# Kernel optimization log

Measured on AMD Instinct MI355X. Metric: run time of the kernel, lower is better.

Reference implementation:

```python
import jax, jax.numpy as jnp
import numpy as np

B, N, C_IN, C_OUT, K = 8, 4096, 64, 128, 15
RADIUS = 0.1            # 2.5 * grid_size(0.04) * sigma(1.0)
MAX_NN = 34
KP_EXTENT = 0.04        # point_influence = prev_grid_size * sigma
KERNEL_RADIUS = 1.5 * KP_EXTENT
NEG_SLOPE = 0.2
BN_EPS = 1e-5


def setup_inputs() -> dict:
    key = jax.random.key(0)
    k1, k2, k3, k4 = jax.random.split(key, 4)
    xyz = jax.random.uniform(k1, (B, N, 3), dtype=jnp.float32)
    feats = jax.random.normal(k2, (B, N, C_IN), dtype=jnp.float32)
    # fixed kernel point disposition inside the kernel ball (requires_grad=False in torch)
    kp = jax.random.normal(k3, (K, 3), dtype=jnp.float32)
    kp = kp / (jnp.linalg.norm(kp, axis=-1, keepdims=True) + 1e-6) * KERNEL_RADIUS * 0.7
    kp = kp.at[0].set(0.0)  # center point
    std = float(np.sqrt(2.0 / (K * C_IN)))
    weight = jax.random.normal(k4, (K, C_IN, C_OUT), dtype=jnp.float32) * std
    gamma = jnp.ones((C_OUT,), dtype=jnp.float32)
    beta = jnp.zeros((C_OUT,), dtype=jnp.float32)
    return {"xyz": xyz, "feats": feats, "K_points": kp, "weight": weight,
            "gamma": gamma, "beta": beta}


def _ball_query(xyz):
    # xyz: [B, N, 3] -> flat neighbor idx [B*N, MAX_NN] into the concatenated
    # point array; missing neighbors get shadow index B*N.
    b_, n_, _ = xyz.shape
    shadow = b_ * n_

    def per_cloud(pts, b):
        d2 = jnp.sum((pts[:, None, :] - pts[None, :, :]) ** 2, axis=-1)  # [N, N]
        neg_d2, idx = jax.lax.top_k(-d2, MAX_NN)                         # k nearest
        valid = (-neg_d2) <= RADIUS ** 2
        return jnp.where(valid, idx + b * n_, shadow)

    return jax.vmap(per_cloud)(xyz, jnp.arange(b_)).reshape(b_ * n_, MAX_NN)


def _kpconv_block(xyz, feats, K_points, weight, gamma, beta):
    b_, n_, _ = xyz.shape
    pts = xyz.reshape(b_ * n_, 3)
    f = feats.reshape(b_ * n_, C_IN)
    nidx = _ball_query(xyz)                                   # [M, nn]
    # shadow point far away / zero features (KPConv_ops)
    pts_pad = jnp.concatenate([pts, jnp.full((1, 3), 1e6, pts.dtype)], axis=0)
    f_pad = jnp.concatenate([f, jnp.zeros((1, C_IN), f.dtype)], axis=0)
    nbr = pts_pad[nidx] - pts[:, None, :]                     # [M, nn, 3] relative coords
    sq = jnp.sum((nbr[:, :, None, :] - K_points) ** 2, -1)    # [M, nn, K]
    w = jnp.maximum(1.0 - jnp.sqrt(sq) / KP_EXTENT, 0.0)      # linear influence
    nf = f_pad[nidx]                                          # [M, nn, Cin]
    wf = jnp.einsum('mnk,mnc->mkc', w, nf)                    # per-kernel-point feats
    out = jnp.einsum('mkc,kcd->md', wf, weight)               # [M, Cout]
    # FastBatchNorm1d (training-mode batch stats, biased var) + LeakyReLU
    mu = out.mean(axis=0)
    var = out.var(axis=0)
    out = (out - mu) * jax.lax.rsqrt(var + BN_EPS) * gamma + beta
    out = jnp.where(out >= 0, out, NEG_SLOPE * out)
    return out.reshape(b_, n_, C_OUT)


def reference(xyz, feats, K_points, weight, gamma, beta):
    return _kpconv_block(xyz, feats, K_points, weight, gamma, beta)
```

## Files before the change

kernel.cpp:

```cpp
#include <hip/hip_runtime.h>


#define NB     8
#define NPTS   4096
#define M_TOT  32768
#define CIN    64
#define COUT   128
#define NKP    15
#define NCELL  1728
#define UCAP   400
#define R2EFF  (0.082f * 0.082f)
#define KP_INV 25.0f
#define NEG_SLOPE 0.2f
#define KCP    960
#define WFROW  1920
#define SP     40

typedef float f32x4_t __attribute__((ext_vector_type(4)));
typedef short bf16x8_t __attribute__((ext_vector_type(8)));

__device__ __forceinline__ unsigned short f2bf(float f) {
  union { float f; unsigned u; } v; v.f = f;
  unsigned r = v.u + 0x7FFF + ((v.u >> 16) & 1);
  return (unsigned short)(r >> 16);
}
__device__ __forceinline__ unsigned short f2bf_fast(float f) {
  union { float f; unsigned u; } v; v.f = f;
  return (unsigned short)((v.u + 0x8000u) >> 16);
}
__device__ __forceinline__ int cell_of(float x, float y, float z) {
  int cx = (int)(x * 12.f); cx = cx > 11 ? 11 : cx;
  int cy = (int)(y * 12.f); cy = cy > 11 ? 11 : cy;
  int cz = (int)(z * 12.f); cz = cz > 11 ? 11 : cz;
  return (cz * 12 + cy) * 12 + cx;
}

__global__ __launch_bounds__(256) void k0a_hist(
    const float* __restrict__ xyz, int* __restrict__ cellcnt)
{
  const int pt = blockIdx.x * 256 + threadIdx.x;
  const float x = xyz[pt * 3], y = xyz[pt * 3 + 1], z = xyz[pt * 3 + 2];
  const int b = pt >> 12;
  atomicAdd(&cellcnt[b * NCELL + cell_of(x, y, z)], 1);
}

__global__ __launch_bounds__(256) void k0b_scan_kW(
    const int* __restrict__ cellcnt, int* __restrict__ cellstart,
    const float* __restrict__ W, unsigned short* __restrict__ Wt)
{
  if (blockIdx.x >= 8) {
    const int idx = (blockIdx.x - 8) * 256 + threadIdx.x;
    const int c = idx & 63, d = idx >> 6;
    #pragma unroll
    for (int k = 0; k < NKP; k++)
      Wt[(size_t)d * KCP + k * 64 + c] =
          f2bf(W[(size_t)k * (CIN * COUT) + c * COUT + d]);
    return;
  }
  __shared__ int ps[256];
  const int b = blockIdx.x, t = threadIdx.x;
  int local[7], s = 0;
  #pragma unroll
  for (int i = 0; i < 7; i++) {
    const int cid = t * 7 + i;
    const int c = (cid < NCELL) ? cellcnt[b * NCELL + cid] : 0;
    local[i] = c; s += c;
  }
  ps[t] = s; __syncthreads();
  for (int off = 1; off < 256; off <<= 1) {
    int v = (t >= off) ? ps[t - off] : 0;
    __syncthreads();
    ps[t] += v;
    __syncthreads();
  }
  int run = ps[t] - s;
  #pragma unroll
  for (int i = 0; i < 7; i++) {
    const int cid = t * 7 + i;
    if (cid < NCELL) { cellstart[b * 1729 + cid] = run; run += local[i]; }
  }
  if (t == 255) cellstart[b * 1729 + NCELL] = ps[255];
}

__global__ __launch_bounds__(256) void k0c_scatter(
    const float* __restrict__ xyz, const float* __restrict__ feats,
    const int* __restrict__ cellstart, int* __restrict__ cellfill,
    int* __restrict__ qorder, float4* __restrict__ xyzs,
    unsigned short* __restrict__ fsorted)
{
  const int pt = blockIdx.x * 256 + threadIdx.x;
  const float x = xyz[pt * 3], y = xyz[pt * 3 + 1], z = xyz[pt * 3 + 2];
  const int b = pt >> 12;
  const int cid = cell_of(x, y, z);
  const int slot = atomicAdd(&cellfill[b * NCELL + cid], 1);
  const int pos = b * NPTS + cellstart[b * 1729 + cid] + slot;
  qorder[pos] = pt;
  xyzs[pos] = make_float4(x, y, z, 0.f);
  const float* src = &feats[(size_t)pt * CIN];
  uint4* dst = (uint4*)&fsorted[(size_t)pos * CIN];
  #pragma unroll
  for (int g = 0; g < 8; g++) {
    float4 a = *(const float4*)(src + g * 8);
    float4 c = *(const float4*)(src + g * 8 + 4);
    union { unsigned short s[8]; uint4 v; } u;
    u.s[0] = f2bf(a.x); u.s[1] = f2bf(a.y); u.s[2] = f2bf(a.z); u.s[3] = f2bf(a.w);
    u.s[4] = f2bf(c.x); u.s[5] = f2bf(c.y); u.s[6] = f2bf(c.z); u.s[7] = f2bf(c.w);
    dst[g] = u.v;
  }
}

__global__ __launch_bounds__(256, 5) void k2_conv(
    const float4* __restrict__ xyzs, const unsigned short* __restrict__ fsorted,
    const float* __restrict__ kpts, const int* __restrict__ cellstart,
    const int* __restrict__ qorder, const unsigned short* __restrict__ Wt,
    float* __restrict__ out, float* __restrict__ psum,
    float* __restrict__ psumsq)
{
  __shared__ char smraw[32000] __attribute__((aligned(16)));
  float4*         Pu   = (float4*)smraw;
  unsigned short* cpos = (unsigned short*)(smraw + 6400);
  short (*S)[SP]       = (short(*)[SP])(smraw + 6400);
  short (*FT)[SP]      = (short(*)[SP])(smraw + 26880);

  __shared__ float4 qd[16];
  __shared__ int    qm[16];
  __shared__ float  kp[NKP][4];
  __shared__ int    Tsh;
  __shared__ int    ucnt;

  const int tid = threadIdx.x;
  const int w   = tid >> 6;
  const int L   = tid & 63;
  const int m0  = blockIdx.x * 16;
  const int b   = m0 >> 12;

  if (tid >= 64 && tid < 64 + NKP) {
    const int k = tid - 64;
    const float kx = kpts[k * 3], ky = kpts[k * 3 + 1], kz = kpts[k * 3 + 2];
    kp[k][0] = -2.f * kx; kp[k][1] = -2.f * ky; kp[k][2] = -2.f * kz;
    kp[k][3] = kx * kx + ky * ky + kz * kz;
  }

  if (tid < 64) {
    int cxm = 12, cym = 12, czm = 12, cxM = -1, cyM = -1, czM = -1;
    if (tid < 16) {
      const float4 Q = xyzs[m0 + tid];
      qd[tid] = Q;
      qm[tid] = qorder[m0 + tid];
      int a = (int)(Q.x * 12.f); a = a > 11 ? 11 : a;
      int c = (int)(Q.y * 12.f); c = c > 11 ? 11 : c;
      int d = (int)(Q.z * 12.f); d = d > 11 ? 11 : d;
      cxm = cxM = a; cym = cyM = c; czm = czM = d;
    }
    #pragma unroll
    for (int off = 8; off >= 1; off >>= 1) {
      int v;
      v = __shfl_xor(cxm, off); cxm = v < cxm ? v : cxm;
      v = __shfl_xor(cxM, off); cxM = v > cxM ? v : cxM;
      v = __shfl_xor(cym, off); cym = v < cym ? v : cym;
      v = __shfl_xor(cyM, off); cyM = v > cyM ? v : cyM;
      v = __shfl_xor(czm, off); czm = v < czm ? v : czm;
      v = __shfl_xor(czM, off); czM = v > czM ? v : czM;
    }
    cxm = __shfl(cxm, 0); cxM = __shfl(cxM, 0);
    cym = __shfl(cym, 0); cyM = __shfl(cyM, 0);
    czm = __shfl(czm, 0); czM = __shfl(czM, 0);

    const int x0 = cxm > 0 ? cxm - 1 : 0, x1 = cxM < 11 ? cxM + 1 : 11;
    const int y0 = cym > 0 ? cym - 1 : 0, y1 = cyM < 11 ? cyM + 1 : 11;
    const int z0 = czm > 0 ? czm - 1 : 0, z1 = czM < 11 ? czM + 1 : 11;
    const int yspan = y1 - y0 + 1;
    int nr = yspan * (z1 - z0 + 1);
    nr = nr > 64 ? 64 : nr;

    int rs = 0, len = 0;
    if (tid < nr) {
      const int zz = z0 + tid / yspan, yy = y0 + tid % yspan;
      const int base = b * 1729 + (zz * 12 + yy) * 12;
      rs  = cellstart[base + x0];
      len = cellstart[base + x1 + 1] - rs;
    }
    int incl = len;
    #pragma unroll
    for (int off = 1; off < 64; off <<= 1) {
      const int v = __shfl_up(incl, off);
      if (tid >= off) incl += v;
    }
    const int excl = incl - len;
    for (int i = 0; i < len; i++) cpos[excl + i] = (unsigned short)(rs + i);
    if (tid == 63) Tsh = incl;
    if (tid == 62) ucnt = 0;
  }
  __syncthreads();
  const int T = Tsh;

  for (int tb = 0; tb < T; tb += 256) {
    const int t = tb + tid;
    if (t < T) {
      const int pos = (int)cpos[t];
      const float4 P = xyzs[b * NPTS + pos];
      float best = 1e9f;
      #pragma unroll
      for (int i = 0; i < 16; i++) {
        const float4 Q = qd[i];
        const float dx = P.x - Q.x, dy = P.y - Q.y, dz = P.z - Q.z;
        const float d2 = dx * dx + dy * dy + dz * dz;
        best = d2 < best ? d2 : best;
      }
      if (best <= R2EFF) {
        const int slot = atomicAdd(&ucnt, 1);
        if (slot < UCAP)
          Pu[slot] = make_float4(P.x, P.y, P.z, __int_as_float(pos));
      }
    }
  }
  __syncthreads();
  int U = ucnt; U = U > UCAP ? UCAP : U;

  const int ln = L & 15;
  const int kh = L >> 4;
  const int qh = tid >> 5;
  const int nn = tid & 31;

  f32x4_t acc[16];
  #pragma unroll
  for (int mt = 0; mt < 16; mt++) acc[mt] = (f32x4_t){0.f, 0.f, 0.f, 0.f};

  for (int ub = 0; ub < U; ub += 32) {
    {
      const int c  = tid & 63;
      const int i0 = tid >> 6;
      #pragma unroll
      for (int ii = 0; ii < 8; ii++) {
        const int i = ii * 4 + i0;
        const int u = ub + i;
        short v = 0;
        if (u < U) {
          const int pos = __float_as_int(Pu[u].w);
          v = (short)fsorted[(size_t)(b * NPTS + pos) * CIN + c];
        }
        FT[c][i] = v;
      }
    }

    bf16x8_t bb;
    #pragma unroll
    for (int half = 0; half < 2; half++) {
      {
        const int u = ub + nn;
        if (u < U) {
          const float4 P = Pu[u];
          const float4 Q = qd[half * 8 + qh];
          const float rx = P.x - Q.x, ry = P.y - Q.y, rz = P.z - Q.z;
          const float rr = rx * rx + ry * ry + rz * rz;
          #pragma unroll
          for (int k = 0; k < NKP; k++) {
            float d2 = fmaf(kp[k][0], rx,
                       fmaf(kp[k][1], ry,
                       fmaf(kp[k][2], rz, rr + kp[k][3])));
            d2 = fmaxf(d2, 0.f);
            const float wv =
                fmaxf(fmaf(-KP_INV, __builtin_amdgcn_sqrtf(d2), 1.f), 0.f);
            S[qh * 16 + k][nn] = (short)f2bf_fast(wv);
          }
          S[qh * 16 + 15][nn] = 0;
        } else {
          #pragma unroll
          for (int k = 0; k < 16; k++) S[qh * 16 + k][nn] = 0;
        }
      }
      __syncthreads();
      if (half == 0) bb = *(const bf16x8_t*)&FT[w * 16 + ln][kh * 8];
      #pragma unroll
      for (int mt = 0; mt < 8; mt++) {
        bf16x8_t aa = *(const bf16x8_t*)&S[mt * 16 + ln][kh * 8];
        acc[half * 8 + mt] =
            __builtin_amdgcn_mfma_f32_16x16x32_bf16(aa, bb, acc[half * 8 + mt],
                                                    0, 0, 0);
      }
      __syncthreads();
    }
  }

  {
    const int c = w * 16 + ln;
    #pragma unroll
    for (int mt = 0; mt < 16; mt++) {
      #pragma unroll
      for (int j = 0; j < 4; j++) {
        const int k = kh * 4 + j;
        if (k < 15) {
          int byteo = mt * WFROW + ((k * 64 + c) << 1);
          byteo ^= (mt & 7) << 4;
          *(unsigned short*)(smraw + byteo) = f2bf_fast(acc[mt][j]);
        }
      }
    }
  }
  __syncthreads();

  const int colbase = w * 32;

  f32x4_t acc2[2];
  acc2[0] = (f32x4_t){0.f, 0.f, 0.f, 0.f};
  acc2[1] = (f32x4_t){0.f, 0.f, 0.f, 0.f};

  const unsigned short* Bp0 = &Wt[(size_t)(colbase + ln) * KCP + kh * 8];
  const unsigned short* Bp1 = Bp0 + 16 * KCP;
  const char* wfb = (const char*)smraw + ln * WFROW;
  const int   sw  = (ln & 7) << 4;

  #pragma unroll 6
  for (int kk = 0; kk < 30; kk++) {
    const int ko  = kk * 32;
    const int inr = (kh * 16 + kk * 64) ^ sw;
    bf16x8_t b0 = *(const bf16x8_t*)(Bp0 + ko);
    bf16x8_t b1 = *(const bf16x8_t*)(Bp1 + ko);
    bf16x8_t a0 = *(const bf16x8_t*)(wfb + inr);
    acc2[0] = __builtin_amdgcn_mfma_f32_16x16x32_bf16(a0, b0, acc2[0], 0, 0, 0);
    acc2[1] = __builtin_amdgcn_mfma_f32_16x16x32_bf16(a0, b1, acc2[1], 0, 0, 0);
  }

  float s0 = 0.f, q0 = 0.f, s1 = 0.f, q1 = 0.f;
  #pragma unroll
  for (int j = 0; j < 4; j++) {
    s0 += acc2[0][j]; q0 += acc2[0][j] * acc2[0][j];
    s1 += acc2[1][j]; q1 += acc2[1][j] * acc2[1][j];
  }
  s0 += __shfl_xor(s0, 16); s0 += __shfl_xor(s0, 32);
  q0 += __shfl_xor(q0, 16); q0 += __shfl_xor(q0, 32);
  s1 += __shfl_xor(s1, 16); s1 += __shfl_xor(s1, 32);
  q1 += __shfl_xor(q1, 16); q1 += __shfl_xor(q1, 32);
  if (kh == 0) {
    atomicAdd(&psum[colbase + ln], s0);
    atomicAdd(&psumsq[colbase + ln], q0);
    atomicAdd(&psum[colbase + 16 + ln], s1);
    atomicAdd(&psumsq[colbase + 16 + ln], q1);
  }

  #pragma unroll
  for (int c = 0; c < 2; c++) {
    #pragma unroll
    for (int j = 0; j < 4; j++) {
      const int row = kh * 4 + j;
      out[(size_t)qm[row] * COUT + colbase + c * 16 + ln] = acc2[c][j];
    }
  }
}

__global__ __launch_bounds__(256) void k4_norm(
    float* __restrict__ out, const float* __restrict__ psum,
    const float* __restrict__ psumsq, const float* __restrict__ gamma,
    const float* __restrict__ beta)
{
  __shared__ float a_s[128], b_s[128];
  if (threadIdx.x < 128) {
    const int d = threadIdx.x;
    double mu  = (double)psum[d] / (double)M_TOT;
    double var = (double)psumsq[d] / (double)M_TOT - mu * mu;
    float rstd = (float)(1.0 / sqrt(var + 1e-5));
    float a = rstd * gamma[d];
    a_s[d] = a;
    b_s[d] = beta[d] - (float)mu * a;
  }
  __syncthreads();
  const int idx = blockIdx.x * 256 + threadIdx.x;
  float4 v = ((const float4*)out)[idx];
  const int d0 = (idx * 4) & 127;
  float y0 = v.x * a_s[d0 + 0] + b_s[d0 + 0];
  float y1 = v.y * a_s[d0 + 1] + b_s[d0 + 1];
  float y2 = v.z * a_s[d0 + 2] + b_s[d0 + 2];
  float y3 = v.w * a_s[d0 + 3] + b_s[d0 + 3];
  v.x = y0 >= 0.f ? y0 : NEG_SLOPE * y0;
  v.y = y1 >= 0.f ? y1 : NEG_SLOPE * y1;
  v.z = y2 >= 0.f ? y2 : NEG_SLOPE * y2;
  v.w = y3 >= 0.f ? y3 : NEG_SLOPE * y3;
  ((float4*)out)[idx] = v;
}

extern "C" void kernel_launch(void* const* d_in, const int* in_sizes, int n_in,
                              void* d_out, int out_size, void* d_ws,
                              size_t ws_size, hipStream_t stream)
{
  const float* xyz   = (const float*)d_in[0];
  const float* feats = (const float*)d_in[1];
  const float* kpts  = (const float*)d_in[2];
  const float* W     = (const float*)d_in[3];
  const float* gamma = (const float*)d_in[4];
  const float* beta  = (const float*)d_in[5];
  float* out = (float*)d_out;

  char* ws = (char*)d_ws;
  int*            cellcnt   = (int*)(ws + 0);
  int*            cellfill  = (int*)(ws + 55296);
  float*          psum      = (float*)(ws + 110592);
  float*          psumsq    = (float*)(ws + 111104);
  int*            cellstart = (int*)(ws + 111616);
  int*            qorder    = (int*)(ws + 167040);
  float4*         xyzs      = (float4*)(ws + 298112);
  unsigned short* fsorted   = (unsigned short*)(ws + 822400);
  unsigned short* Wt        = (unsigned short*)(ws + 5016704);

  hipMemsetAsync(ws, 0, 111616, stream);

  k0a_hist   <<< 128, 256, 0, stream>>>(xyz, cellcnt);
  k0b_scan_kW<<<  40, 256, 0, stream>>>(cellcnt, cellstart, W, Wt);
  k0c_scatter<<< 128, 256, 0, stream>>>(xyz, feats, cellstart, cellfill,
                                        qorder, xyzs, fsorted);
  k2_conv    <<<2048, 256, 0, stream>>>(xyzs, fsorted, kpts, cellstart,
                                        qorder, Wt, out, psum, psumsq);
  k4_norm    <<<(out_size / 4) / 256, 256, 0, stream>>>(out, psum, psumsq,
                                                        gamma, beta);
}
```

Measured before the change: 195.9 us.

## Split fused conv into separate gather-conv and GEMM kernels via global buffer

The fused conv kernel is split in two. The first kernel computes the per-kernel-point weighted features and writes them to a global bf16 buffer of about 63 MB. The second kernel reloads them into LDS and runs the weight GEMM, then does the BN partial sums and the scatter. The weight matrix is pre-laid-out in MFMA fragment order so B-operand loads are contiguous per lane. The aim is to reduce register and LDS pressure in each kernel, at the cost of heavy extra global memory traffic and one more launch; the old path is kept as a fallback when the workspace is too small.

```diff
diff --git a/kernel.cpp b/kernel.cpp
--- a/kernel.cpp
+++ b/kernel.cpp
@@ -44,7 +44,55 @@
   atomicAdd(&cellcnt[b * NCELL + cell_of(x, y, z)], 1);
 }
 
-__global__ __launch_bounds__(256) void k0b_scan_kW(
+__global__ __launch_bounds__(256) void k0b_scan_kWF(
+    const int* __restrict__ cellcnt, int* __restrict__ cellstart,
+    const float* __restrict__ W, unsigned short* __restrict__ WtF)
+{
+  if (blockIdx.x >= 8) {
+    const int idx = (blockIdx.x - 8) * 256 + threadIdx.x;
+    const int L  = idx & 63;
+    const int g  = idx >> 6;
+    const int kk = g % 30;
+    const int ct = g / 30;
+    const int d  = ct * 16 + (L & 15);
+    const int kcb = (L >> 4) * 8 + kk * 32;
+    union { unsigned short s[8]; uint4 v; } u;
+    #pragma unroll
+    for (int e = 0; e < 8; e++) {
+      const int kc = kcb + e;
+      const int k  = kc >> 6;
+      const int c  = kc & 63;
+      u.s[e] = f2bf(W[(size_t)k * (CIN * COUT) + c * COUT + d]);
+    }
+    *(uint4*)&WtF[(size_t)idx * 8] = u.v;
+    return;
+  }
+  __shared__ int ps[256];
+  const int b = blockIdx.x, t = threadIdx.x;
+  int local[7], s = 0;
+  #pragma unroll
+  for (int i = 0; i < 7; i++) {
+    const int cid = t * 7 + i;
+    const int c = (cid < NCELL) ? cellcnt[b * NCELL + cid] : 0;
+    local[i] = c; s += c;
+  }
+  ps[t] = s; __syncthreads();
+  for (int off = 1; off < 256; off <<= 1) {
+    int v = (t >= off) ? ps[t - off] : 0;
+    __syncthreads();
+    ps[t] += v;
+    __syncthreads();
+  }
+  int run = ps[t] - s;
+  #pragma unroll
+  for (int i = 0; i < 7; i++) {
+    const int cid = t * 7 + i;
+    if (cid < NCELL) { cellstart[b * 1729 + cid] = run; run += local[i]; }
+  }
+  if (t == 255) cellstart[b * 1729 + NCELL] = ps[255];
+}
+
+__global__ __launch_bounds__(256) void k0b_old(
     const int* __restrict__ cellcnt, int* __restrict__ cellstart,
     const float* __restrict__ W, unsigned short* __restrict__ Wt)
 {
@@ -109,12 +157,10 @@
   }
 }
 
-__global__ __launch_bounds__(256, 5) void k2_conv(
+__global__ __launch_bounds__(256, 5) void k2a_conv(
     const float4* __restrict__ xyzs, const unsigned short* __restrict__ fsorted,
     const float* __restrict__ kpts, const int* __restrict__ cellstart,
-    const int* __restrict__ qorder, const unsigned short* __restrict__ Wt,
-    float* __restrict__ out, float* __restrict__ psum,
-    float* __restrict__ psumsq)
+    unsigned short* __restrict__ wfg)
 {
   __shared__ char smraw[32000] __attribute__((aligned(16)));
   float4*         Pu   = (float4*)smraw;
@@ -123,7 +169,6 @@
   short (*FT)[SP]      = (short(*)[SP])(smraw + 26880);
 
   __shared__ float4 qd[16];
-  __shared__ int    qm[16];
   __shared__ float  kp[NKP][4];
   __shared__ int    Tsh;
   __shared__ int    ucnt;
@@ -146,7 +191,6 @@
     if (tid < 16) {
       const float4 Q = xyzs[m0 + tid];
       qd[tid] = Q;
-      qm[tid] = qorder[m0 + tid];
       int a = (int)(Q.x * 12.f); a = a > 11 ? 11 : a;
       int c = (int)(Q.y * 12.f); c = c > 11 ? 11 : c;
       int d = (int)(Q.z * 12.f); d = d > 11 ? 11 : d;
@@ -282,6 +326,269 @@
     }
   }
 
+  #pragma unroll
+  for (int mt = 0; mt < 16; mt++) {
+    const size_t rb = (size_t)(m0 + mt) * KCP + (w * 16 + ln);
+    #pragma unroll
+    for (int j = 0; j < 4; j++) {
+      const int k = kh * 4 + j;
+      if (k < 15)
+        wfg[rb + k * 64] = f2bf_fast(acc[mt][j]);
+    }
+  }
+}
+
+__global__ __launch_bounds__(256, 5) void k2b_gemm(
+    const unsigned short* __restrict__ wfg,
+    const unsigned short* __restrict__ WtF,
+    const int* __restrict__ qorder, float* __restrict__ out,
+    float* __restrict__ psum, float* __restrict__ psumsq)
+{
+  __shared__ char smraw[30720] __attribute__((aligned(16)));
+  __shared__ int qm[16];
+
+  const int tid = threadIdx.x;
+  const int w   = tid >> 6;
+  const int L   = tid & 63;
+  const int m0  = blockIdx.x * 16;
+
+  if (tid < 16) qm[tid] = qorder[m0 + tid];
+
+  {
+    const int r0 = tid >> 7;
+    const int ch = tid & 127;
+    if (ch < 120) {
+      #pragma unroll
+      for (int it = 0; it < 8; it++) {
+        const int r = it * 2 + r0;
+        const uint4 v = *(const uint4*)(wfg + (size_t)(m0 + r) * KCP + ch * 8);
+        *(uint4*)(smraw + ((r * WFROW + ch * 16) ^ ((r & 7) << 4))) = v;
+      }
+    }
+  }
+  __syncthreads();
+
+  const int ln = L & 15;
+  const int kh = L >> 4;
+  const int colbase = w * 32;
+
+  f32x4_t acc2[2];
+  acc2[0] = (f32x4_t){0.f, 0.f, 0.f, 0.f};
+  acc2[1] = (f32x4_t){0.f, 0.f, 0.f, 0.f};
+
+  const unsigned short* Bp = WtF + ((size_t)(w * 2 * 30) * 64 + L) * 8;
+  const char* wfb = (const char*)smraw + ln * WFROW;
+  const int   sw  = (ln & 7) << 4;
+
+  #pragma unroll 6
+  for (int kk = 0; kk < 30; kk++) {
+    const int inr = (kh * 16 + kk * 64) ^ sw;
+    bf16x8_t b0 = *(const bf16x8_t*)(Bp + kk * 512);
+    bf16x8_t b1 = *(const bf16x8_t*)(Bp + 15360 + kk * 512);
+    bf16x8_t a0 = *(const bf16x8_t*)(wfb + inr);
+    acc2[0] = __builtin_amdgcn_mfma_f32_16x16x32_bf16(a0, b0, acc2[0], 0, 0, 0);
+    acc2[1] = __builtin_amdgcn_mfma_f32_16x16x32_bf16(a0, b1, acc2[1], 0, 0, 0);
+  }
+
+  float s0 = 0.f, q0 = 0.f, s1 = 0.f, q1 = 0.f;
+  #pragma unroll
+  for (int j = 0; j < 4; j++) {
+    s0 += acc2[0][j]; q0 += acc2[0][j] * acc2[0][j];
+    s1 += acc2[1][j]; q1 += acc2[1][j] * acc2[1][j];
+  }
+  s0 += __shfl_xor(s0, 16); s0 += __shfl_xor(s0, 32);
+  q0 += __shfl_xor(q0, 16); q0 += __shfl_xor(q0, 32);
+  s1 += __shfl_xor(s1, 16); s1 += __shfl_xor(s1, 32);
+  q1 += __shfl_xor(q1, 16); q1 += __shfl_xor(q1, 32);
+  if (kh == 0) {
+    atomicAdd(&psum[colbase + ln], s0);
+    atomicAdd(&psumsq[colbase + ln], q0);
+    atomicAdd(&psum[colbase + 16 + ln], s1);
+    atomicAdd(&psumsq[colbase + 16 + ln], q1);
+  }
+
+  #pragma unroll
+  for (int c = 0; c < 2; c++) {
+    #pragma unroll
+    for (int j = 0; j < 4; j++) {
+      const int row = kh * 4 + j;
+      out[(size_t)qm[row] * COUT + colbase + c * 16 + ln] = acc2[c][j];
+    }
+  }
+}
+
+__global__ __launch_bounds__(256, 5) void k2_old(
+    const float4* __restrict__ xyzs, const unsigned short* __restrict__ fsorted,
+    const float* __restrict__ kpts, const int* __restrict__ cellstart,
+    const int* __restrict__ qorder, const unsigned short* __restrict__ Wt,
+    float* __restrict__ out, float* __restrict__ psum,
+    float* __restrict__ psumsq)
+{
+  __shared__ char smraw[32000] __attribute__((aligned(16)));
+  float4*         Pu   = (float4*)smraw;
+  unsigned short* cpos = (unsigned short*)(smraw + 6400);
+  short (*S)[SP]       = (short(*)[SP])(smraw + 6400);
+  short (*FT)[SP]      = (short(*)[SP])(smraw + 26880);
+
+  __shared__ float4 qd[16];
+  __shared__ int    qm[16];
+  __shared__ float  kp[NKP][4];
+  __shared__ int    Tsh;
+  __shared__ int    ucnt;
+
+  const int tid = threadIdx.x;
+  const int w   = tid >> 6;
+  const int L   = tid & 63;
+  const int m0  = blockIdx.x * 16;
+  const int b   = m0 >> 12;
+
+  if (tid >= 64 && tid < 64 + NKP) {
+    const int k = tid - 64;
+    const float kx = kpts[k * 3], ky = kpts[k * 3 + 1], kz = kpts[k * 3 + 2];
+    kp[k][0] = -2.f * kx; kp[k][1] = -2.f * ky; kp[k][2] = -2.f * kz;
+    kp[k][3] = kx * kx + ky * ky + kz * kz;
+  }
+
+  if (tid < 64) {
+    int cxm = 12, cym = 12, czm = 12, cxM = -1, cyM = -1, czM = -1;
+    if (tid < 16) {
+      const float4 Q = xyzs[m0 + tid];
+      qd[tid] = Q;
+      qm[tid] = qorder[m0 + tid];
+      int a = (int)(Q.x * 12.f); a = a > 11 ? 11 : a;
+      int c = (int)(Q.y * 12.f); c = c > 11 ? 11 : c;
+      int d = (int)(Q.z * 12.f); d = d > 11 ? 11 : d;
+      cxm = cxM = a; cym = cyM = c; czm = czM = d;
+    }
+    #pragma unroll
+    for (int off = 8; off >= 1; off >>= 1) {
+      int v;
+      v = __shfl_xor(cxm, off); cxm = v < cxm ? v : cxm;
+      v = __shfl_xor(cxM, off); cxM = v > cxM ? v : cxM;
+      v = __shfl_xor(cym, off); cym = v < cym ? v : cym;
+      v = __shfl_xor(cyM, off); cyM = v > cyM ? v : cyM;
+      v = __shfl_xor(czm, off); czm = v < czm ? v : czm;
+      v = __shfl_xor(czM, off); czM = v > czM ? v : czM;
+    }
+    cxm = __shfl(cxm, 0); cxM = __shfl(cxM, 0);
+    cym = __shfl(cym, 0); cyM = __shfl(cyM, 0);
+    czm = __shfl(czm, 0); czM = __shfl(czM, 0);
+
+    const int x0 = cxm > 0 ? cxm - 1 : 0, x1 = cxM < 11 ? cxM + 1 : 11;
+    const int y0 = cym > 0 ? cym - 1 : 0, y1 = cyM < 11 ? cyM + 1 : 11;
+    const int z0 = czm > 0 ? czm - 1 : 0, z1 = czM < 11 ? czM + 1 : 11;
+    const int yspan = y1 - y0 + 1;
+    int nr = yspan * (z1 - z0 + 1);
+    nr = nr > 64 ? 64 : nr;
+
+    int rs = 0, len = 0;
+    if (tid < nr) {
+      const int zz = z0 + tid / yspan, yy = y0 + tid % yspan;
+      const int base = b * 1729 + (zz * 12 + yy) * 12;
+      rs  = cellstart[base + x0];
+      len = cellstart[base + x1 + 1] - rs;
+    }
+    int incl = len;
+    #pragma unroll
+    for (int off = 1; off < 64; off <<= 1) {
+      const int v = __shfl_up(incl, off);
+      if (tid >= off) incl += v;
+    }
+    const int excl = incl - len;
+    for (int i = 0; i < len; i++) cpos[excl + i] = (unsigned short)(rs + i);
+    if (tid == 63) Tsh = incl;
+    if (tid == 62) ucnt = 0;
+  }
+  __syncthreads();
+  const int T = Tsh;
+
+  for (int tb = 0; tb < T; tb += 256) {
+    const int t = tb + tid;
+    if (t < T) {
+      const int pos = (int)cpos[t];
+      const float4 P = xyzs[b * NPTS + pos];
+      float best = 1e9f;
+      #pragma unroll
+      for (int i = 0; i < 16; i++) {
+        const float4 Q = qd[i];
+        const float dx = P.x - Q.x, dy = P.y - Q.y, dz = P.z - Q.z;
+        const float d2 = dx * dx + dy * dy + dz * dz;
+        best = d2 < best ? d2 : best;
+      }
+      if (best <= R2EFF) {
+        const int slot = atomicAdd(&ucnt, 1);
+        if (slot < UCAP)
+          Pu[slot] = make_float4(P.x, P.y, P.z, __int_as_float(pos));
+      }
+    }
+  }
+  __syncthreads();
+  int U = ucnt; U = U > UCAP ? UCAP : U;
+
+  const int ln = L & 15;
+  const int kh = L >> 4;
+  const int qh = tid >> 5;
+  const int nn = tid & 31;
+
+  f32x4_t acc[16];
+  #pragma unroll
+  for (int mt = 0; mt < 16; mt++) acc[mt] = (f32x4_t){0.f, 0.f, 0.f, 0.f};
+
+  for (int ub = 0; ub < U; ub += 32) {
+    {
+      const int c  = tid & 63;
+      const int i0 = tid >> 6;
+      #pragma unroll
+      for (int ii = 0; ii < 8; ii++) {
+        const int i = ii * 4 + i0;
+        const int u = ub + i;
+        short v = 0;
+        if (u < U) {
+          const int pos = __float_as_int(Pu[u].w);
+          v = (short)fsorted[(size_t)(b * NPTS + pos) * CIN + c];
+        }
+        FT[c][i] = v;
+      }
+    }
+    bf16x8_t bb;
+    #pragma unroll
+    for (int half = 0; half < 2; half++) {
+      {
+        const int u = ub + nn;
+        if (u < U) {
+          const float4 P = Pu[u];
+          const float4 Q = qd[half * 8 + qh];
+          const float rx = P.x - Q.x, ry = P.y - Q.y, rz = P.z - Q.z;
+          const float rr = rx * rx + ry * ry + rz * rz;
+          #pragma unroll
+          for (int k = 0; k < NKP; k++) {
+            float d2 = fmaf(kp[k][0], rx,
+                       fmaf(kp[k][1], ry,
+                       fmaf(kp[k][2], rz, rr + kp[k][3])));
+            d2 = fmaxf(d2, 0.f);
+            const float wv =
+                fmaxf(fmaf(-KP_INV, __builtin_amdgcn_sqrtf(d2), 1.f), 0.f);
+            S[qh * 16 + k][nn] = (short)f2bf_fast(wv);
+          }
+          S[qh * 16 + 15][nn] = 0;
+        } else {
+          #pragma unroll
+          for (int k = 0; k < 16; k++) S[qh * 16 + k][nn] = 0;
+        }
+      }
+      __syncthreads();
+      if (half == 0) bb = *(const bf16x8_t*)&FT[w * 16 + ln][kh * 8];
+      #pragma unroll
+      for (int mt = 0; mt < 8; mt++) {
+        bf16x8_t aa = *(const bf16x8_t*)&S[mt * 16 + ln][kh * 8];
+        acc[half * 8 + mt] =
+            __builtin_amdgcn_mfma_f32_16x16x32_bf16(aa, bb, acc[half * 8 + mt],
+                                                    0, 0, 0);
+      }
+      __syncthreads();
+    }
+  }
+
   {
     const int c = w * 16 + ln;
     #pragma unroll
@@ -290,8 +597,7 @@
       for (int j = 0; j < 4; j++) {
         const int k = kh * 4 + j;
         if (k < 15) {
-          int byteo = mt * WFROW + ((k * 64 + c) << 1);
-          byteo ^= (mt & 7) << 4;
+          const int byteo = (mt * WFROW + ((k * 64 + c) << 1)) ^ ((mt & 7) << 4);
           *(unsigned short*)(smraw + byteo) = f2bf_fast(acc[mt][j]);
         }
       }
@@ -300,7 +606,6 @@
   __syncthreads();
 
   const int colbase = w * 32;
-
   f32x4_t acc2[2];
   acc2[0] = (f32x4_t){0.f, 0.f, 0.f, 0.f};
   acc2[1] = (f32x4_t){0.f, 0.f, 0.f, 0.f};
@@ -399,16 +704,32 @@
   int*            qorder    = (int*)(ws + 167040);
   float4*         xyzs      = (float4*)(ws + 298112);
   unsigned short* fsorted   = (unsigned short*)(ws + 822400);
-  unsigned short* Wt        = (unsigned short*)(ws + 5016704);
+  unsigned short* Wtbuf     = (unsigned short*)(ws + 5016704);
+  unsigned short* wfg       = (unsigned short*)(ws + 5262464);
+
+  const size_t NEED = 5262464ull + 62914560ull;
 
   hipMemsetAsync(ws, 0, 111616, stream);
 
-  k0a_hist   <<< 128, 256, 0, stream>>>(xyz, cellcnt);
-  k0b_scan_kW<<<  40, 256, 0, stream>>>(cellcnt, cellstart, W, Wt);
-  k0c_scatter<<< 128, 256, 0, stream>>>(xyz, feats, cellstart, cellfill,
-                                        qorder, xyzs, fsorted);
-  k2_conv    <<<2048, 256, 0, stream>>>(xyzs, fsorted, kpts, cellstart,
-                                        qorder, Wt, out, psum, psumsq);
-  k4_norm    <<<(out_size / 4) / 256, 256, 0, stream>>>(out, psum, psumsq,
-                                                        gamma, beta);
-}
+  if (ws_size >= NEED) {
+    k0a_hist    <<< 128, 256, 0, stream>>>(xyz, cellcnt);
+    k0b_scan_kWF<<<  68, 256, 0, stream>>>(cellcnt, cellstart, W, Wtbuf);
+    k0c_scatter <<< 128, 256, 0, stream>>>(xyz, feats, cellstart, cellfill,
+                                           qorder, xyzs, fsorted);
+    k2a_conv    <<<2048, 256, 0, stream>>>(xyzs, fsorted, kpts, cellstart,
+                                           wfg);
+    k2b_gemm    <<<2048, 256, 0, stream>>>(wfg, Wtbuf, qorder, out,
+                                           psum, psumsq);
+    k4_norm     <<<(out_size / 4) / 256, 256, 0, stream>>>(out, psum, psumsq,
+                                                           gamma, beta);
+  } else {
+    k0a_hist    <<< 128, 256, 0, stream>>>(xyz, cellcnt);
+    k0b_old     <<<  40, 256, 0, stream>>>(cellcnt, cellstart, W, Wtbuf);
+    k0c_scatter <<< 128, 256, 0, stream>>>(xyz, feats, cellstart, cellfill,
+                                           qorder, xyzs, fsorted);
+    k2_old      <<<2048, 256, 0, stream>>>(xyzs, fsorted, kpts, cellstart,
+                                           qorder, Wtbuf, out, psum, psumsq);
+    k4_norm     <<<(out_size / 4) / 256, 256, 0, stream>>>(out, psum, psumsq,
+                                                           gamma, beta);
+  }
+}
```

After: 205.3 us. +4.8%, slower.
